# Kernel tuning notes

Hardware: AMD Instinct MI355X
Metric: run time of the kernel (lower is better)

Reference implementation:

```python
import jax, jax.numpy as jnp
import numpy as np


def setup_inputs() -> dict:
    key = jax.random.key(0)
    k1, k2 = jax.random.split(key)
    V, K, C = 200000, 64, 4
    coords = jax.random.normal(k1, (V, C), dtype=jnp.float32)
    nidx = jax.random.randint(k2, (V, K), 0, V, dtype=jnp.int32)
    return {"coords": coords, "nidx": nidx}


def reference(coords, nidx):
    # SelectWithDefault: gather coords at nidx, using 0.0 where nidx < 0
    valid = nidx >= 0                              # [V, K]
    safe_idx = jnp.where(valid, nidx, 0)
    ncoords = coords[safe_idx]                     # [V, K, C]
    ncoords = jnp.where(valid[..., None], ncoords, 0.0)
    # squared distance to own coordinates
    diff = ncoords - coords[:, None, :]            # [V, K, C]
    dist = jnp.sum(diff * diff, axis=2)            # [V, K]
    return dist
```

## Files before the change

kernel.cpp:

```cpp
#include <hip/hip_runtime.h>


__global__ __launch_bounds__(256) void RecalcDistances_kernel(
    const float4* __restrict__ coords,
    const int4*   __restrict__ nidx,
    float4*       __restrict__ out,
    int total_groups,
    int groups_per_row)
{
    int tid = blockIdx.x * blockDim.x + threadIdx.x;
    if (tid >= total_groups) return;

    int v = tid / groups_per_row;
    float4 c = coords[v];
    int4 idx = nidx[tid];

    float4 r;
    {
        float4 n = (idx.x >= 0) ? coords[idx.x] : make_float4(0.f, 0.f, 0.f, 0.f);
        float dx = n.x - c.x, dy = n.y - c.y, dz = n.z - c.z, dw = n.w - c.w;
        r.x = dx * dx + dy * dy + dz * dz + dw * dw;
    }
    {
        float4 n = (idx.y >= 0) ? coords[idx.y] : make_float4(0.f, 0.f, 0.f, 0.f);
        float dx = n.x - c.x, dy = n.y - c.y, dz = n.z - c.z, dw = n.w - c.w;
        r.y = dx * dx + dy * dy + dz * dz + dw * dw;
    }
    {
        float4 n = (idx.z >= 0) ? coords[idx.z] : make_float4(0.f, 0.f, 0.f, 0.f);
        float dx = n.x - c.x, dy = n.y - c.y, dz = n.z - c.z, dw = n.w - c.w;
        r.z = dx * dx + dy * dy + dz * dz + dw * dw;
    }
    {
        float4 n = (idx.w >= 0) ? coords[idx.w] : make_float4(0.f, 0.f, 0.f, 0.f);
        float dx = n.x - c.x, dy = n.y - c.y, dz = n.z - c.z, dw = n.w - c.w;
        r.w = dx * dx + dy * dy + dz * dz + dw * dw;
    }

    out[tid] = r;
}

extern "C" void kernel_launch(void* const* d_in, const int* in_sizes, int n_in,
                              void* d_out, int out_size, void* d_ws, size_t ws_size,
                              hipStream_t stream) {
    const float4* coords = (const float4*)d_in[0];
    const int4*   nidx   = (const int4*)d_in[1];
    float4*       out    = (float4*)d_out;

    const int C = 4;
    int V = in_sizes[0] / C;
    int K = in_sizes[1] / V;
    int groups_per_row = K / 4;
    int total_groups = V * groups_per_row;

    int block = 256;
    int grid = (total_groups + block - 1) / block;
    RecalcDistances_kernel<<<grid, block, 0, stream>>>(coords, nidx, out,
                                                       total_groups, groups_per_row);
}
```

Measured before the change: 62.20 us.

## Process two index groups per thread with streaming loads and branchless gathers

Each thread now handles two int4 index groups, one stride apart, and issues all eight coordinate gathers before any arithmetic. The aim is to keep more random loads in flight to hide gather latency. Index reads and output writes use nontemporal loads and stores so the streamed data does not evict the coords table from cache. The per-thread division becomes a shift, and invalid indices are clamped to 0 and masked after the load, which replaces divergent branches. The shift is only correct when the groups per row is a power of two, and a specialised template drops the bounds checks when the sizes divide exactly.

```diff
diff --git a/kernel.cpp b/kernel.cpp
--- a/kernel.cpp
+++ b/kernel.cpp
@@ -1,51 +1,69 @@
 #include <hip/hip_runtime.h>
 
 
+typedef int   vint4   __attribute__((ext_vector_type(4)));
+typedef float vfloat4 __attribute__((ext_vector_type(4)));
+
+__device__ __forceinline__ float sqdist(vfloat4 n, vfloat4 c, bool valid) {
+    n = valid ? n : (vfloat4)(0.f, 0.f, 0.f, 0.f);
+    float dx = n.x - c.x, dy = n.y - c.y, dz = n.z - c.z, dw = n.w - c.w;
+    return dx * dx + dy * dy + dz * dz + dw * dw;
+}
+
+template<bool EXACT>
 __global__ __launch_bounds__(256) void RecalcDistances_kernel(
-    const float4* __restrict__ coords,
-    const int4*   __restrict__ nidx,
-    float4*       __restrict__ out,
+    const vfloat4* __restrict__ coords,
+    const vint4*   __restrict__ nidx,
+    vfloat4*       __restrict__ out,
     int total_groups,
-    int groups_per_row)
+    int shift,
+    int stride)
 {
     int tid = blockIdx.x * blockDim.x + threadIdx.x;
-    if (tid >= total_groups) return;
+    int g0 = tid;
+    int g1 = tid + stride;
 
-    int v = tid / groups_per_row;
-    float4 c = coords[v];
-    int4 idx = nidx[tid];
+    bool ok1 = EXACT || (g1 < total_groups);
+    if (!EXACT && g0 >= total_groups) return;
 
-    float4 r;
-    {
-        float4 n = (idx.x >= 0) ? coords[idx.x] : make_float4(0.f, 0.f, 0.f, 0.f);
-        float dx = n.x - c.x, dy = n.y - c.y, dz = n.z - c.z, dw = n.w - c.w;
-        r.x = dx * dx + dy * dy + dz * dz + dw * dw;
-    }
-    {
-        float4 n = (idx.y >= 0) ? coords[idx.y] : make_float4(0.f, 0.f, 0.f, 0.f);
-        float dx = n.x - c.x, dy = n.y - c.y, dz = n.z - c.z, dw = n.w - c.w;
-        r.y = dx * dx + dy * dy + dz * dz + dw * dw;
-    }
-    {
-        float4 n = (idx.z >= 0) ? coords[idx.z] : make_float4(0.f, 0.f, 0.f, 0.f);
-        float dx = n.x - c.x, dy = n.y - c.y, dz = n.z - c.z, dw = n.w - c.w;
-        r.z = dx * dx + dy * dy + dz * dz + dw * dw;
-    }
-    {
-        float4 n = (idx.w >= 0) ? coords[idx.w] : make_float4(0.f, 0.f, 0.f, 0.f);
-        float dx = n.x - c.x, dy = n.y - c.y, dz = n.z - c.z, dw = n.w - c.w;
-        r.w = dx * dx + dy * dy + dz * dz + dw * dw;
-    }
+    vint4 i0 = __builtin_nontemporal_load(&nidx[g0]);
+    vint4 i1 = ok1 ? __builtin_nontemporal_load(&nidx[g1]) : (vint4)(0, 0, 0, 0);
+    vfloat4 c0 = coords[g0 >> shift];
+    vfloat4 c1 = coords[(ok1 ? g1 : g0) >> shift];
 
-    out[tid] = r;
+    int s00 = max(i0.x, 0), s01 = max(i0.y, 0), s02 = max(i0.z, 0), s03 = max(i0.w, 0);
+    int s10 = max(i1.x, 0), s11 = max(i1.y, 0), s12 = max(i1.z, 0), s13 = max(i1.w, 0);
+
+    vfloat4 n00 = coords[s00];
+    vfloat4 n01 = coords[s01];
+    vfloat4 n02 = coords[s02];
+    vfloat4 n03 = coords[s03];
+    vfloat4 n10 = coords[s10];
+    vfloat4 n11 = coords[s11];
+    vfloat4 n12 = coords[s12];
+    vfloat4 n13 = coords[s13];
+
+    vfloat4 r0;
+    r0.x = sqdist(n00, c0, i0.x >= 0);
+    r0.y = sqdist(n01, c0, i0.y >= 0);
+    r0.z = sqdist(n02, c0, i0.z >= 0);
+    r0.w = sqdist(n03, c0, i0.w >= 0);
+    __builtin_nontemporal_store(r0, &out[g0]);
+
+    vfloat4 r1;
+    r1.x = sqdist(n10, c1, i1.x >= 0);
+    r1.y = sqdist(n11, c1, i1.y >= 0);
+    r1.z = sqdist(n12, c1, i1.z >= 0);
+    r1.w = sqdist(n13, c1, i1.w >= 0);
+    if (ok1) __builtin_nontemporal_store(r1, &out[g1]);
 }
 
 extern "C" void kernel_launch(void* const* d_in, const int* in_sizes, int n_in,
                               void* d_out, int out_size, void* d_ws, size_t ws_size,
                               hipStream_t stream) {
-    const float4* coords = (const float4*)d_in[0];
-    const int4*   nidx   = (const int4*)d_in[1];
-    float4*       out    = (float4*)d_out;
+    const vfloat4* coords = (const vfloat4*)d_in[0];
+    const vint4*   nidx   = (const vint4*)d_in[1];
+    vfloat4*       out    = (vfloat4*)d_out;
 
     const int C = 4;
     int V = in_sizes[0] / C;
@@ -53,8 +71,21 @@
     int groups_per_row = K / 4;
     int total_groups = V * groups_per_row;
 
+    int shift = 0;
+    while ((1 << shift) < groups_per_row) ++shift;
+
+    const int ILP = 2;
     int block = 256;
-    int grid = (total_groups + block - 1) / block;
-    RecalcDistances_kernel<<<grid, block, 0, stream>>>(coords, nidx, out,
-                                                       total_groups, groups_per_row);
+    int nthreads = (total_groups + ILP - 1) / ILP;
+    int grid = (nthreads + block - 1) / block;
+    int stride = grid * block;
+
+    bool exact = (total_groups == 2 * stride) && ((1 << shift) == groups_per_row);
+    if (exact) {
+        RecalcDistances_kernel<true><<<grid, block, 0, stream>>>(
+            coords, nidx, out, total_groups, shift, stride);
+    } else {
+        RecalcDistances_kernel<false><<<grid, block, 0, stream>>>(
+            coords, nidx, out, total_groups, shift, stride);
+    }
 }
```

Measured after the change: 66.24 us. 1.06x slower.
